# Performance work log

Hardware: AMD Instinct MI355X
Metric: run time of the kernel (lower is better)

## Reference

```python
import jax, jax.numpy as jnp
import numpy as np

D_IN = 1024
D_OUT = 1024
NUM_HEADS = 16
HEAD_DIM = D_OUT // NUM_HEADS
SEQ = 2048
BATCH = 2


def setup_inputs() -> dict:
    key = jax.random.key(0)
    ks = jax.random.split(key, 6)
    s = 1.0 / np.sqrt(D_IN)
    x = jax.random.normal(ks[0], (BATCH, SEQ, D_IN), dtype=jnp.float32)
    Wq = jax.random.uniform(ks[1], (D_IN, D_OUT), jnp.float32, -s, s)
    Wk = jax.random.uniform(ks[2], (D_IN, D_OUT), jnp.float32, -s, s)
    Wv = jax.random.uniform(ks[3], (D_IN, D_OUT), jnp.float32, -s, s)
    Wo = jax.random.uniform(ks[4], (D_OUT, D_OUT), jnp.float32, -s, s)
    bo = jax.random.uniform(ks[5], (D_OUT,), jnp.float32, -s, s)
    return {"x": x, "Wq": Wq, "Wk": Wk, "Wv": Wv, "Wo": Wo, "bo": bo}


def reference(x, Wq, Wk, Wv, Wo, bo):
    b, n, _ = x.shape
    # projections, split into heads: (b, h, n, hd)
    def split_heads(t):
        return t.reshape(b, n, NUM_HEADS, HEAD_DIM).transpose(0, 2, 1, 3)
    q = split_heads(x @ Wq)
    k = split_heads(x @ Wk)
    v = split_heads(x @ Wv)
    scores = jnp.einsum("bhqd,bhkd->bhqk", q, k)
    causal = jnp.triu(jnp.ones((n, n), dtype=bool), k=1)
    scores = jnp.where(causal, -jnp.inf, scores)
    attn = jax.nn.softmax(scores / np.sqrt(HEAD_DIM), axis=-1)
    # dropout prob is 0.0 -> identity
    ctx = jnp.einsum("bhqk,bhkd->bhqd", attn, v)
    ctx = ctx.transpose(0, 2, 1, 3).reshape(b, n, D_OUT)
    return ctx @ Wo + bo
```

## Files before the change

### kernel.cpp

```cpp
#include <hip/hip_runtime.h>
#include <hip/hip_bf16.h>
#include <stdint.h>

#define D_IN   1024
#define D_OUT  1024
#define NHEAD  16
#define HDIM   64
#define SEQ    2048
#define BATCH  2
#define M_TOT  (BATCH*SEQ)

typedef __attribute__((ext_vector_type(8)))  short bfx8;
typedef __attribute__((ext_vector_type(4)))  short bfx4;
typedef __attribute__((ext_vector_type(4)))  float fx4;
typedef __attribute__((ext_vector_type(16))) float fx16;
typedef unsigned short u16;
typedef unsigned int   u32;

__device__ __forceinline__ u16 f2bf(float f) {
    u32 u = __builtin_bit_cast(u32, f);
    u32 r = (u + 0x7FFFu + ((u >> 16) & 1u)) >> 16;
    return (u16)r;
}
__device__ __forceinline__ float bf2f(u16 v) {
    u32 u = (u32)v << 16;
    return __builtin_bit_cast(float, u);
}

__device__ __forceinline__ u32 cvtpk(float lo, float hi) {
    u32 r;
    asm("v_cvt_pk_bf16_f32 %0, %1, %2" : "=v"(r) : "v"(lo), "v"(hi));
    return r;
}

__device__ __forceinline__ float exp2x(float x) {
    float r;
    asm("v_exp_f32 %0, %1" : "=v"(r) : "v"(x));
    return r;
}

__device__ __forceinline__ void gload16(const u16* g, u16* l) {
    __builtin_amdgcn_global_load_lds(
        (const __attribute__((address_space(1))) void*)g,
        (__attribute__((address_space(3))) void*)l, 16, 0, 0);
}

__global__ void k_conv(const float* __restrict__ x,
                       const float* __restrict__ Wq, const float* __restrict__ Wk,
                       const float* __restrict__ Wv, const float* __restrict__ Wo,
                       u16* __restrict__ xb, u16* __restrict__ wt) {
    __shared__ float tile[32][33];
    const int bid = blockIdx.x;
    if (bid < 2048) {
        int i = bid * 256 + threadIdx.x;
        const float4* s = reinterpret_cast<const float4*>(x);
        float4 a = s[2*i], b = s[2*i+1];
        uint4 o;
        o.x = (u32)f2bf(a.x) | ((u32)f2bf(a.y) << 16);
        o.y = (u32)f2bf(a.z) | ((u32)f2bf(a.w) << 16);
        o.z = (u32)f2bf(b.x) | ((u32)f2bf(b.y) << 16);
        o.w = (u32)f2bf(b.z) | ((u32)f2bf(b.w) << 16);
        reinterpret_cast<uint4*>(xb)[i] = o;
        return;
    }
    const int b2 = bid - 2048;
    const int wsel = b2 >> 10, rem = b2 & 1023;
    const int by = rem >> 5, bx = rem & 31;
    const float* W = (wsel == 0) ? Wq : (wsel == 1) ? Wk : (wsel == 2) ? Wv : Wo;
    const float scale = (wsel == 0) ? 0.125f * 1.4426950408889634f : 1.0f;
    u16* dst = wt + (size_t)wsel * D_IN * D_OUT;
    int r0 = by * 32, c0 = bx * 32;
    int tx = threadIdx.x & 31, ty = threadIdx.x >> 5;
    #pragma unroll
    for (int k = 0; k < 4; k++) {
        int i = ty + k * 8;
        tile[i][tx] = W[(size_t)(r0 + i) * D_OUT + c0 + tx];
    }
    __syncthreads();
    #pragma unroll
    for (int k = 0; k < 4; k++) {
        int i = ty + k * 8;
        dst[(size_t)(c0 + i) * D_IN + r0 + tx] = f2bf(tile[tx][i] * scale);
    }
}

__global__ __launch_bounds__(256) void k_qkv(const u16* __restrict__ A,
                                             const u16* __restrict__ Bt,
                                             u16* __restrict__ outb) {
    __shared__ u16 aL[128][32];
    __shared__ u16 bL[128][32];
    __shared__ u16 tb[64][132];
    const int K = 1024;
    const int nb = blockIdx.x * 128, mb = blockIdx.y * 128;
    const int t = threadIdx.x, lane = t & 63, w = t >> 6;
    const int wr = w >> 1, wc = w & 1;
    const int li = lane & 15, lg = lane >> 4;
    const int srow = lane >> 2, schunk = (lane & 3) * 8;

    fx4 acc[4][4];
    #pragma unroll
    for (int i = 0; i < 4; i++)
        #pragma unroll
        for (int j = 0; j < 4; j++) acc[i][j] = fx4{0.f, 0.f, 0.f, 0.f};

    const u16* aBase = A  + (size_t)(mb + w * 32 + srow) * K + schunk;
    const u16* bBase = Bt + (size_t)(nb + w * 32 + srow) * K + schunk;

    for (int kb = 0; kb < K; kb += 32) {
        #pragma unroll
        for (int c = 0; c < 2; c++) {
            gload16(aBase + (size_t)c * 16 * K + kb, &aL[w * 32 + c * 16][0]);
            gload16(bBase + (size_t)c * 16 * K + kb, &bL[w * 32 + c * 16][0]);
        }
        __syncthreads();
        bfx8 af[4], bf[4];
        #pragma unroll
        for (int mi = 0; mi < 4; mi++)
            af[mi] = *reinterpret_cast<const bfx8*>(&aL[wr * 64 + mi * 16 + li][lg * 8]);
        #pragma unroll
        for (int ni = 0; ni < 4; ni++)
            bf[ni] = *reinterpret_cast<const bfx8*>(&bL[wc * 64 + ni * 16 + li][lg * 8]);
        #pragma unroll
        for (int mi = 0; mi < 4; mi++)
            #pragma unroll
            for (int ni = 0; ni < 4; ni++)
                acc[mi][ni] = __builtin_amdgcn_mfma_f32_16x16x32_bf16(af[mi], bf[ni], acc[mi][ni], 0, 0, 0);
        __syncthreads();
    }

    if (nb < 2048) {
        #pragma unroll
        for (int mi = 0; mi < 4; mi++) {
            #pragma unroll
            for (int ni = 0; ni < 4; ni++) {
                const int n = nb + wc * 64 + ni * 16 + li;
                const int m0 = mb + wr * 64 + mi * 16 + lg * 4;
                const int proj = n >> 10, h = (n >> 6) & 15, d = n & 63;
                const int b = m0 >> 11, s0 = m0 & 2047;
                u16* op = outb + (size_t)proj * M_TOT * D_OUT;
                #pragma unroll
                for (int r = 0; r < 4; r++)
                    op[((size_t)(b * NHEAD + h) * SEQ + s0 + r) * HDIM + d] =
                        f2bf(acc[mi][ni][r]);
            }
        }
    } else {
        const int b = mb >> 11, sb = mb & 2047;
        const int h0 = (nb - 2048) >> 6;
        u16* vt = outb + (size_t)2 * M_TOT * D_OUT;
        #pragma unroll
        for (int hf = 0; hf < 2; hf++) {
            if (wc == hf) {
                #pragma unroll
                for (int ni = 0; ni < 4; ni++) {
                    const int d = ni * 16 + li;
                    #pragma unroll
                    for (int mi = 0; mi < 4; mi++) {
                        const int m0 = wr * 64 + mi * 16 + lg * 4;
                        bfx4 pk = {(short)f2bf(acc[mi][ni][0]), (short)f2bf(acc[mi][ni][1]),
                                   (short)f2bf(acc[mi][ni][2]), (short)f2bf(acc[mi][ni][3])};
                        *reinterpret_cast<bfx4*>(&tb[d][m0]) = pk;
                    }
                }
            }
            __syncthreads();
            const int h = h0 + hf;
            const int d = lane;
            u16* vrow = vt + (((size_t)(b * NHEAD + h) * HDIM + d) * SEQ) + sb;
            #pragma unroll
            for (int i = 0; i < 4; i++) {
                const int j = w + i * 4;
                *reinterpret_cast<bfx8*>(&vrow[j * 8]) =
                    *reinterpret_cast<const bfx8*>(&tb[d][j * 8]);
            }
            __syncthreads();
        }
    }
}

__global__ __launch_bounds__(256) void k_oproj(const u16* __restrict__ A,
                                               const u16* __restrict__ Bt,
                                               const float* __restrict__ bias,
                                               float* __restrict__ outf) {
    __shared__ u16 aL[128][32];
    __shared__ u16 bL[64][32];
    const int K = 1024;
    const int nb = blockIdx.x * 64, mb = blockIdx.y * 128;
    const int t = threadIdx.x, lane = t & 63, w = t >> 6;
    const int wr = w >> 1, wc = w & 1;
    const int li = lane & 15, lg = lane >> 4;
    const int srow = lane >> 2, schunk = (lane & 3) * 8;

    fx4 acc[4][2];
    #pragma unroll
    for (int i = 0; i < 4; i++)
        #pragma unroll
        for (int j = 0; j < 2; j++) acc[i][j] = fx4{0.f, 0.f, 0.f, 0.f};

    const u16* aBase = A  + (size_t)(mb + w * 32 + srow) * K + schunk;
    const u16* bBase = Bt + (size_t)(nb + w * 16 + srow) * K + schunk;

    for (int kb = 0; kb < K; kb += 32) {
        gload16(aBase + kb,          &aL[w * 32][0]);
        gload16(aBase + 16 * K + kb, &aL[w * 32 + 16][0]);
        gload16(bBase + kb,          &bL[w * 16][0]);
        __syncthreads();
        bfx8 af[4], bf[2];
        #pragma unroll
        for (int mi = 0; mi < 4; mi++)
            af[mi] = *reinterpret_cast<const bfx8*>(&aL[wr * 64 + mi * 16 + li][lg * 8]);
        #pragma unroll
        for (int ni = 0; ni < 2; ni++)
            bf[ni] = *reinterpret_cast<const bfx8*>(&bL[wc * 32 + ni * 16 + li][lg * 8]);
        #pragma unroll
        for (int mi = 0; mi < 4; mi++)
            #pragma unroll
            for (int ni = 0; ni < 2; ni++)
                acc[mi][ni] = __builtin_amdgcn_mfma_f32_16x16x32_bf16(af[mi], bf[ni], acc[mi][ni], 0, 0, 0);
        __syncthreads();
    }

    #pragma unroll
    for (int mi = 0; mi < 4; mi++) {
        #pragma unroll
        for (int ni = 0; ni < 2; ni++) {
            const int n = nb + wc * 32 + ni * 16 + li;
            const int m0 = mb + wr * 64 + mi * 16 + lg * 4;
            const float bv = bias[n];
            #pragma unroll
            for (int r = 0; r < 4; r++)
                outf[(size_t)(m0 + r) * D_OUT + n] = acc[mi][ni][r] + bv;
        }
    }
}

__global__ __launch_bounds__(512, 2) void k_attn(const u16* __restrict__ Q,
                                                 const u16* __restrict__ Kp,
                                                 const u16* __restrict__ Vt,
                                                 u16* __restrict__ ctx,
                                                 u16* __restrict__ o1,
                                                 float* __restrict__ l0,
                                                 float* __restrict__ l1) {
    __shared__ u16 kbuf[3][64][64];
    __shared__ u16 vbuf[3][64][64];

    static const __constant__ signed char QT[12]   = {7,7,6,6,5,5,4,4,3,2,1,0};
    static const __constant__ signed char PART[12] = {0,1,0,1,0,1,0,1,0,0,0,0};

    const int g  = blockIdx.x;
    const int m  = g & 31, pp = g >> 5;
    const int bh = (m & 7) * 4 + (m >> 3);
    const int qt = QT[pp], part = PART[pp];
    const bool heavy = (qt >= 4);
    const int nt = 4 * qt + 4;
    int t0, t1;
    if (heavy) { int h1 = nt >> 1; t0 = part ? h1 : 0; t1 = part ? nt : h1; }
    else       { t0 = 0; t1 = nt; }
    const int ntL = t1 - t0;

    const size_t base = (size_t)bh * SEQ * HDIM;
    const int t = threadIdx.x, lane = t & 63, w = t >> 6;
    const int l31 = lane & 31, hi = lane >> 5;
    const int srow = lane >> 3;
    const int ts = (lane & 7) ^ srow;
    const int bq = bh >> 4, hh = bh & 15;
    const int swz = (l31 & 7) * 8;
    const int qwb = qt * 256 + w * 32;
    const int qg  = qwb + l31;

    auto stage = [&](int bi, int kvb) {
        const int rb = w * 8;
        gload16(Kp + base + (size_t)(kvb + rb + srow) * HDIM + ts * 8,
                &kbuf[bi][rb][0]);
        gload16(Vt + base + (size_t)(rb + srow) * SEQ + kvb + ts * 8,
                &vbuf[bi][rb][0]);
    };

    bfx8 qf[4];
    #pragma unroll
    for (int dc = 0; dc < 4; dc++)
        qf[dc] = *reinterpret_cast<const bfx8*>(
            &Q[base + (size_t)qg * HDIM + dc * 16 + hi * 8]);
    fx16 cacc[2];
    #pragma unroll
    for (int dt = 0; dt < 2; dt++)
        #pragma unroll
        for (int r = 0; r < 16; r++) cacc[dt][r] = 0.f;
    float lsum = 0.f;

    stage(0, t0 * 64);
    if (ntL > 1) stage(1, (t0 + 1) * 64);

    for (int tt = 0; tt < ntL; tt++) {
        const int ti = t0 + tt, kvb = ti * 64;
        if (tt + 1 < ntL) {
            asm volatile("s_waitcnt vmcnt(2)" ::: "memory");
        } else {
            asm volatile("s_waitcnt vmcnt(0)" ::: "memory");
        }
        __builtin_amdgcn_s_barrier();
        __builtin_amdgcn_sched_barrier(0);
        const int bi = tt % 3;
        if (kvb <= qwb + 31) {
            fx16 sc[2];
            __builtin_amdgcn_s_setprio(1);
            #pragma unroll
            for (int s = 0; s < 2; s++) {
                #pragma unroll
                for (int r = 0; r < 16; r++) sc[s][r] = 0.f;
                #pragma unroll
                for (int dc = 0; dc < 4; dc++) {
                    bfx8 kf = *reinterpret_cast<const bfx8*>(
                        &kbuf[bi][s * 32 + l31][(dc * 16 + hi * 8) ^ swz]);
                    sc[s] = __builtin_amdgcn_mfma_f32_32x32x16_bf16(kf, qf[dc], sc[s], 0, 0, 0);
                }
            }
            __builtin_amdgcn_s_setprio(0);
            if (kvb + 63 > qwb) {
                #pragma unroll
                for (int s = 0; s < 2; s++)
                    #pragma unroll
                    for (int r = 0; r < 16; r++) {
                        int kvg = kvb + s * 32 + (r & 3) + 8 * (r >> 2) + 4 * hi;
                        if (kvg > qg) sc[s][r] = -1e30f;
                    }
            }
            float ps = 0.f;
            #pragma unroll
            for (int s = 0; s < 2; s++)
                #pragma unroll
                for (int r = 0; r < 16; r++) {
                    float pv = exp2x(sc[s][r]);
                    sc[s][r] = pv;
                    ps += pv;
                }
            lsum += ps;
            #pragma unroll
            for (int c = 0; c < 4; c++) {
                const int s = c >> 1, rb_ = (c & 1) * 8;
                u32 a0 = cvtpk(sc[s][rb_ + 0], sc[s][rb_ + 1]);
                u32 a1 = cvtpk(sc[s][rb_ + 2], sc[s][rb_ + 3]);
                u32 b0 = cvtpk(sc[s][rb_ + 4], sc[s][rb_ + 5]);
                u32 b1 = cvtpk(sc[s][rb_ + 6], sc[s][rb_ + 7]);
                u32 X0 = hi ? a0 : b0, X1 = hi ? a1 : b1;
                u32 Y0 = (u32)__shfl_xor((int)X0, 32);
                u32 Y1 = (u32)__shfl_xor((int)X1, 32);
                uint4 pw;
                pw.x = hi ? Y0 : a0;
                pw.y = hi ? Y1 : a1;
                pw.z = hi ? b0 : Y0;
                pw.w = hi ? b1 : Y1;
                bfx8 pf = __builtin_bit_cast(bfx8, pw);
                __builtin_amdgcn_s_setprio(1);
                #pragma unroll
                for (int dt = 0; dt < 2; dt++) {
                    bfx8 vf = *reinterpret_cast<const bfx8*>(
                        &vbuf[bi][dt * 32 + l31][(c * 16 + hi * 8) ^ swz]);
                    cacc[dt] = __builtin_amdgcn_mfma_f32_32x32x16_bf16(pf, vf, cacc[dt], 0, 0, 0);
                }
                __builtin_amdgcn_s_setprio(0);
            }
        }
        if (tt + 2 < ntL) stage((tt + 2) % 3, (ti + 2) * 64);
    }

    float ltot = lsum + __shfl_xor(lsum, 32);
    if (!heavy) {
        float linv = 1.0f / ltot;
        #pragma unroll
        for (int r = 0; r < 16; r++) {
            const int qpat = (r & 3) + 8 * (r >> 2) + 4 * hi;
            float rl = __shfl(linv, qpat);
            const int q = qwb + qpat;
            #pragma unroll
            for (int dt = 0; dt < 2; dt++)
                ctx[((size_t)(bq * SEQ + q)) * D_OUT + hh * HDIM + dt * 32 + l31] =
                    f2bf(cacc[dt][r] * rl);
        }
    } else {
        const int qt4 = qt - 4;
        const int rbase = (qt4 * 32 + bh) * 256 + w * 32;
        if (hi == 0) { (part ? l1 : l0)[rbase + l31] = ltot; }
        #pragma unroll
        for (int r = 0; r < 16; r++) {
            const int qpat = (r & 3) + 8 * (r >> 2) + 4 * hi;
            const int q = qwb + qpat;
            #pragma unroll
            for (int dt = 0; dt < 2; dt++) {
                const int d = dt * 32 + l31;
                u16 val = f2bf(cacc[dt][r]);
                if (part == 0)
                    ctx[((size_t)(bq * SEQ + q)) * D_OUT + hh * HDIM + d] = val;
                else
                    o1[((size_t)(rbase + qpat)) * 64 + d] = val;
            }
        }
    }
}

__global__ void k_comb(u16* __restrict__ ctx, const u16* __restrict__ o1,
                       const float* __restrict__ l0, const float* __restrict__ l1) {
    int i = blockIdx.x * 256 + threadIdx.x;
    const int d    = (i & 7) * 8;
    const int qrow = (i >> 3) & 255;
    const int bi_  = i >> 11;
    const int bh   = bi_ & 31, qt4 = bi_ >> 5;
    const int bq = bh >> 4, hh = bh & 15;
    const int token = bq * SEQ + (4 + qt4) * 256 + qrow;
    const size_t cidx = (size_t)token * D_OUT + hh * HDIM + d;
    const int ridx = bi_ * 256 + qrow;
    const size_t oidx = (size_t)ridx * 64 + d;
    const float linv = 1.0f / (l0[ridx] + l1[ridx]);
    bfx8 a = *reinterpret_cast<const bfx8*>(&ctx[cidx]);
    bfx8 b = *reinterpret_cast<const bfx8*>(&o1[oidx]);
    bfx8 o;
    #pragma unroll
    for (int j = 0; j < 8; j++)
        o[j] = (short)f2bf((bf2f((u16)a[j]) + bf2f((u16)b[j])) * linv);
    *reinterpret_cast<bfx8*>(&ctx[cidx]) = o;
}

extern "C" void kernel_launch(void* const* d_in, const int* in_sizes, int n_in,
                              void* d_out, int out_size, void* d_ws, size_t ws_size,
                              hipStream_t stream) {
    const float* x  = (const float*)d_in[0];
    const float* Wq = (const float*)d_in[1];
    const float* Wk = (const float*)d_in[2];
    const float* Wv = (const float*)d_in[3];
    const float* Wo = (const float*)d_in[4];
    const float* bo = (const float*)d_in[5];
    float* out = (float*)d_out;

    char* ws = (char*)d_ws;
    u16* xb   = (u16*)(ws);
    u16* wt   = (u16*)(ws + (8u << 20));
    u16* qkvb = (u16*)(ws + (16u << 20));
    u16* ctxb = (u16*)(ws + (40u << 20));

    u16*   o1p = (u16*)(ws);
    float* l0p = (float*)(ws + (4u << 20));
    float* l1p = (float*)(ws + (4u << 20) + (128u << 10));

    const u16* Qb  = qkvb;
    const u16* Kb  = qkvb + (size_t)M_TOT * D_OUT;
    const u16* Vtb = qkvb + (size_t)2 * M_TOT * D_OUT;

    k_conv  <<<6144, 256, 0, stream>>>(x, Wq, Wk, Wv, Wo, xb, wt);
    k_qkv   <<<dim3(24, 32), 256, 0, stream>>>(xb, wt, qkvb);
    k_attn  <<<dim3(384), 512, 0, stream>>>(Qb, Kb, Vtb, ctxb, o1p, l0p, l1p);
    k_comb  <<<1024, 256, 0, stream>>>(ctxb, o1p, l0p, l1p);
    k_oproj <<<dim3(16, 32), 256, 0, stream>>>(
        ctxb, wt + (size_t)3 * D_IN * D_OUT, bo, out);
}
```

Before: 109.3 us.

## Rebalance causal attention work with finer KV splits and ordered scheduling

Causal attention blocks are re-partitioned through lookup tables. Q tiles 7 and 6 now split into three KV chunks, tiles 5 to 3 into two, and the heaviest pieces are dispatched first through an ORDER table, giving 480 work groups instead of 384. The combine kernel now merges two or three partial outputs per row using the new slot layout. The aim is to cut tail imbalance across CUs, at the cost of more partial-result traffic and a larger combine pass.

```diff
diff --git a/kernel.cpp b/kernel.cpp
--- a/kernel.cpp
+++ b/kernel.cpp
@@ -238,24 +238,23 @@
                                                  const u16* __restrict__ Kp,
                                                  const u16* __restrict__ Vt,
                                                  u16* __restrict__ ctx,
-                                                 u16* __restrict__ o1,
-                                                 float* __restrict__ l0,
-                                                 float* __restrict__ l1) {
+                                                 u16* __restrict__ oE,
+                                                 float* __restrict__ l0v,
+                                                 float* __restrict__ lE) {
     __shared__ u16 kbuf[3][64][64];
     __shared__ u16 vbuf[3][64][64];
 
-    static const __constant__ signed char QT[12]   = {7,7,6,6,5,5,4,4,3,2,1,0};
-    static const __constant__ signed char PART[12] = {0,1,0,1,0,1,0,1,0,0,0,0};
+    static const __constant__ signed char PPQT[15]   = {7,7,7,6,6,6,5,5,4,4,3,3,2,1,0};
+    static const __constant__ signed char PPT0[15]   = {0,11,22,0,10,19,0,12,0,10,0,8,0,0,0};
+    static const __constant__ signed char PPT1[15]   = {11,22,32,10,19,28,12,24,10,20,8,16,12,8,4};
+    static const __constant__ signed char PPPART[15] = {0,1,2,0,1,2,0,1,0,1,0,1,0,0,0};
+    static const __constant__ signed char ORDER[15]  = {6,7,12,0,1,2,3,8,9,4,5,10,11,13,14};
 
     const int g  = blockIdx.x;
-    const int m  = g & 31, pp = g >> 5;
+    const int m  = g & 31, pp = ORDER[g >> 5];
     const int bh = (m & 7) * 4 + (m >> 3);
-    const int qt = QT[pp], part = PART[pp];
-    const bool heavy = (qt >= 4);
-    const int nt = 4 * qt + 4;
-    int t0, t1;
-    if (heavy) { int h1 = nt >> 1; t0 = part ? h1 : 0; t1 = part ? nt : h1; }
-    else       { t0 = 0; t1 = nt; }
+    const int qt = PPQT[pp], part = PPPART[pp];
+    const int t0 = PPT0[pp], t1 = PPT1[pp];
     const int ntL = t1 - t0;
 
     const size_t base = (size_t)bh * SEQ * HDIM;
@@ -365,7 +364,7 @@
     }
 
     float ltot = lsum + __shfl_xor(lsum, 32);
-    if (!heavy) {
+    if (qt <= 2) {
         float linv = 1.0f / ltot;
         #pragma unroll
         for (int r = 0; r < 16; r++) {
@@ -377,46 +376,64 @@
                 ctx[((size_t)(bq * SEQ + q)) * D_OUT + hh * HDIM + dt * 32 + l31] =
                     f2bf(cacc[dt][r] * rl);
         }
-    } else {
-        const int qt4 = qt - 4;
-        const int rbase = (qt4 * 32 + bh) * 256 + w * 32;
-        if (hi == 0) { (part ? l1 : l0)[rbase + l31] = ltot; }
+    } else if (part == 0) {
+        if (hi == 0) l0v[((bh * 5 + qt - 3) << 8) + w * 32 + l31] = ltot;
         #pragma unroll
         for (int r = 0; r < 16; r++) {
             const int qpat = (r & 3) + 8 * (r >> 2) + 4 * hi;
             const int q = qwb + qpat;
             #pragma unroll
-            for (int dt = 0; dt < 2; dt++) {
-                const int d = dt * 32 + l31;
-                u16 val = f2bf(cacc[dt][r]);
-                if (part == 0)
-                    ctx[((size_t)(bq * SEQ + q)) * D_OUT + hh * HDIM + d] = val;
-                else
-                    o1[((size_t)(rbase + qpat)) * 64 + d] = val;
-            }
-        }
-    }
-}
-
-__global__ void k_comb(u16* __restrict__ ctx, const u16* __restrict__ o1,
-                       const float* __restrict__ l0, const float* __restrict__ l1) {
+            for (int dt = 0; dt < 2; dt++)
+                ctx[((size_t)(bq * SEQ + q)) * D_OUT + hh * HDIM + dt * 32 + l31] =
+                    f2bf(cacc[dt][r]);
+        }
+    } else {
+        const int slot = (qt == 7) ? (part - 1) : (qt == 6) ? (1 + part)
+                        : (qt == 5) ? 4 : (qt == 4) ? 5 : 6;
+        const int rbase = ((bh * 7 + slot) << 8);
+        if (hi == 0) lE[rbase + w * 32 + l31] = ltot;
+        #pragma unroll
+        for (int r = 0; r < 16; r++) {
+            const int qpat = (r & 3) + 8 * (r >> 2) + 4 * hi;
+            #pragma unroll
+            for (int dt = 0; dt < 2; dt++)
+                oE[((size_t)(rbase + w * 32 + qpat)) * 64 + dt * 32 + l31] =
+                    f2bf(cacc[dt][r]);
+        }
+    }
+}
+
+__global__ void k_comb(u16* __restrict__ ctx, const u16* __restrict__ oE,
+                       const float* __restrict__ l0v, const float* __restrict__ lE) {
     int i = blockIdx.x * 256 + threadIdx.x;
     const int d    = (i & 7) * 8;
-    const int qrow = (i >> 3) & 255;
-    const int bi_  = i >> 11;
-    const int bh   = bi_ & 31, qt4 = bi_ >> 5;
+    const int row  = (i >> 3) & 255;
+    const int idx  = i >> 11;
+    const int bh   = idx / 5, qq = idx - bh * 5;
+    const int qt   = qq + 3;
     const int bq = bh >> 4, hh = bh & 15;
-    const int token = bq * SEQ + (4 + qt4) * 256 + qrow;
-    const size_t cidx = (size_t)token * D_OUT + hh * HDIM + d;
-    const int ridx = bi_ * 256 + qrow;
-    const size_t oidx = (size_t)ridx * 64 + d;
-    const float linv = 1.0f / (l0[ridx] + l1[ridx]);
+    const int slot1 = (qt == 7) ? 0 : (qt == 6) ? 2 : (qt == 5) ? 4 : (qt == 4) ? 5 : 6;
+    const bool three = (qt >= 6);
+    const int q = qt * 256 + row;
+    const size_t cidx = ((size_t)(bq * SEQ + q)) * D_OUT + hh * HDIM + d;
+    const int r1 = ((bh * 7 + slot1) << 8) + row;
+    float l = l0v[((bh * 5 + qq) << 8) + row] + lE[r1];
     bfx8 a = *reinterpret_cast<const bfx8*>(&ctx[cidx]);
-    bfx8 b = *reinterpret_cast<const bfx8*>(&o1[oidx]);
+    bfx8 b = *reinterpret_cast<const bfx8*>(&oE[(size_t)r1 * 64 + d]);
+    float acc[8];
+    #pragma unroll
+    for (int j = 0; j < 8; j++) acc[j] = bf2f((u16)a[j]) + bf2f((u16)b[j]);
+    if (three) {
+        const int r2 = r1 + 256;
+        l += lE[r2];
+        bfx8 c = *reinterpret_cast<const bfx8*>(&oE[(size_t)r2 * 64 + d]);
+        #pragma unroll
+        for (int j = 0; j < 8; j++) acc[j] += bf2f((u16)c[j]);
+    }
+    const float linv = 1.0f / l;
     bfx8 o;
     #pragma unroll
-    for (int j = 0; j < 8; j++)
-        o[j] = (short)f2bf((bf2f((u16)a[j]) + bf2f((u16)b[j])) * linv);
+    for (int j = 0; j < 8; j++) o[j] = (short)f2bf(acc[j] * linv);
     *reinterpret_cast<bfx8*>(&ctx[cidx]) = o;
 }
 
@@ -437,9 +454,9 @@
     u16* qkvb = (u16*)(ws + (16u << 20));
     u16* ctxb = (u16*)(ws + (40u << 20));
 
-    u16*   o1p = (u16*)(ws);
-    float* l0p = (float*)(ws + (4u << 20));
-    float* l1p = (float*)(ws + (4u << 20) + (128u << 10));
+    u16*   oEp = (u16*)(ws);
+    float* l0p = (float*)(ws + 7340032);
+    float* lEp = (float*)(ws + 7503872);
 
     const u16* Qb  = qkvb;
     const u16* Kb  = qkvb + (size_t)M_TOT * D_OUT;
@@ -447,8 +464,8 @@
 
     k_conv  <<<6144, 256, 0, stream>>>(x, Wq, Wk, Wv, Wo, xb, wt);
     k_qkv   <<<dim3(24, 32), 256, 0, stream>>>(xb, wt, qkvb);
-    k_attn  <<<dim3(384), 512, 0, stream>>>(Qb, Kb, Vtb, ctxb, o1p, l0p, l1p);
-    k_comb  <<<1024, 256, 0, stream>>>(ctxb, o1p, l0p, l1p);
+    k_attn  <<<dim3(480), 512, 0, stream>>>(Qb, Kb, Vtb, ctxb, oEp, l0p, lEp);
+    k_comb  <<<1280, 256, 0, stream>>>(ctxb, oEp, l0p, lEp);
     k_oproj <<<dim3(16, 32), 256, 0, stream>>>(
         ctxb, wt + (size_t)3 * D_IN * D_OUT, bo, out);
 }
```

Result: faster. 100.9 us (-7.7%).
